# Optimization experiments

Hardware: AMD Instinct MI355X
Metric: run time of the kernel (lower is better)

## Reference

```python
import jax, jax.numpy as jnp
import numpy as np

TEMPERATURE = 1.0  # init kwarg
B, D = 8192, 128


def setup_inputs() -> dict:
    key = jax.random.key(0)
    k1, k2 = jax.random.split(key)
    sk = jax.random.normal(k1, (B, D), dtype=jnp.float32)
    im = jax.random.normal(k2, (B, D), dtype=jnp.float32)
    return {"sk": sk, "im": im}


def reference(sk, im):
    # The torch module builds a [2B,2B] Euclidean distance matrix over the
    # interleaved [sk_0, im_0, sk_1, im_1, ...] rows, then via the eye-mask /
    # repeat_interleave / [:,1::2] / good_indices / [::2] gather chain selects,
    # for each anchor i, logits row = [-d(sk_i, im_i)/T] ++ [-d(sk_i, im_j)/T, j != i]
    # with label 0, followed by mean cross-entropy.  Since cross-entropy only
    # depends on {row values} and which entry is positive, this is exactly:
    #   loss = mean_i( logsumexp_j(-d(sk_i, im_j)/T) - (-d(sk_i, im_i)/T) )
    # so we only need the [B,B] sk-vs-im distance block (dist_type == 0).
    sq = (
        jnp.sum(sk * sk, axis=1)[:, None]
        + jnp.sum(im * im, axis=1)[None, :]
        - 2.0 * (sk @ im.T)
    )  # [B, B] squared distances
    d = jnp.sqrt(jnp.maximum(sq, 0.0))
    logits = -d / TEMPERATURE  # [B, B]
    lse = jax.nn.logsumexp(logits, axis=1)  # [B]
    loss = jnp.mean(lse - jnp.diagonal(logits))
    return loss
```

## Files before the change

kernel.cpp:

```cpp
#include <hip/hip_runtime.h>
#include <math.h>

#define NB 8192
#define ND 128
#define GSTEP 64
#define NSTEP 8
#define NJB 16

#define C2F 2.0813689810056077f
#define NC2 (-4.1627379620112154f)

typedef float f32x4 __attribute__((ext_vector_type(4)));
typedef unsigned long long ull;

__global__ void __launch_bounds__(256) prep_kernel(
    const float* __restrict__ sk, const float* __restrict__ im,
    ull* __restrict__ skf, ull* __restrict__ imf,
    float* __restrict__ skn, float* __restrict__ imn,
    float* __restrict__ diag, float* __restrict__ gacc,
    unsigned* __restrict__ ticket) {
    if (blockIdx.x == 0 && threadIdx.x == 0) { *gacc = 0.f; *ticket = 0u; }
    const int gtid = blockIdx.x * 256 + threadIdx.x;
    const int row = gtid >> 4;
    const int j = gtid & 15;
    const size_t off = (size_t)row * ND + j * 8;
    const float4* a4 = reinterpret_cast<const float4*>(sk + off);
    const float4* b4 = reinterpret_cast<const float4*>(im + off);
    float4 a0 = a4[0], a1 = a4[1], b0 = b4[0], b1 = b4[1];

    unsigned al = 0, ah = 0, bl = 0, bh = 0;
    al = __builtin_amdgcn_cvt_pk_fp8_f32(a0.x, a0.y, al, false);
    al = __builtin_amdgcn_cvt_pk_fp8_f32(a0.z, a0.w, al, true);
    ah = __builtin_amdgcn_cvt_pk_fp8_f32(a1.x, a1.y, ah, false);
    ah = __builtin_amdgcn_cvt_pk_fp8_f32(a1.z, a1.w, ah, true);
    bl = __builtin_amdgcn_cvt_pk_fp8_f32(b0.x, b0.y, bl, false);
    bl = __builtin_amdgcn_cvt_pk_fp8_f32(b0.z, b0.w, bl, true);
    bh = __builtin_amdgcn_cvt_pk_fp8_f32(b1.x, b1.y, bh, false);
    bh = __builtin_amdgcn_cvt_pk_fp8_f32(b1.z, b1.w, bh, true);

    const size_t didx = (size_t)(row >> 4) * 256 + (j >> 2) * 64 + (j & 3) * 16 + (row & 15);
    skf[didx] = (ull)al | ((ull)ah << 32);
    imf[didx] = (ull)bl | ((ull)bh << 32);

    float sa = a0.x*a0.x + a0.y*a0.y + a0.z*a0.z + a0.w*a0.w
             + a1.x*a1.x + a1.y*a1.y + a1.z*a1.z + a1.w*a1.w;
    float sb = b0.x*b0.x + b0.y*b0.y + b0.z*b0.z + b0.w*b0.w
             + b1.x*b1.x + b1.y*b1.y + b1.z*b1.z + b1.w*b1.w;
    float d0 = a0.x-b0.x, d1 = a0.y-b0.y, d2 = a0.z-b0.z, d3 = a0.w-b0.w;
    float d4 = a1.x-b1.x, d5 = a1.y-b1.y, d6 = a1.z-b1.z, d7 = a1.w-b1.w;
    float sd = d0*d0 + d1*d1 + d2*d2 + d3*d3 + d4*d4 + d5*d5 + d6*d6 + d7*d7;
#pragma unroll
    for (int st = 1; st < 16; st <<= 1) {
        sa += __shfl_xor(sa, st);
        sb += __shfl_xor(sb, st);
        sd += __shfl_xor(sd, st);
    }
    if (j == 0) {
        skn[row] = sa * C2F;
        imn[row] = sb * C2F;
        diag[row] = sqrtf(sd);
    }
}

__global__ void __launch_bounds__(256, 4) tile_kernel(
    const ull* __restrict__ skf, const ull* __restrict__ imf,
    const float* __restrict__ skn, const float* __restrict__ imn,
    float* __restrict__ partial) {
    const int w = threadIdx.x >> 6, lane = threadIdx.x & 63;
    const int hi = lane >> 4, lo = lane & 15;
    const int gw = blockIdx.x * 4 + w;
    const int iw = (gw & 255) * 32;
    const int jgrp = gw >> 8;
    const int jg0 = jgrp * (GSTEP * NSTEP);

    long bfr[2][4];
    const int gi = iw >> 4;
#pragma unroll
    for (int n = 0; n < 2; ++n)
#pragma unroll
        for (int kk = 0; kk < 4; ++kk)
            bfr[n][kk] = (long)skf[(size_t)(gi + n) * 256 + kk * 64 + lane];
    float skv[2];
#pragma unroll
    for (int n = 0; n < 2; ++n) skv[n] = skn[iw + n * 16 + lo];

    float sacc[2] = {0.f, 0.f};

    for (int s = 0; s < NSTEP; ++s) {
        const int jb = jg0 + s * GSTEP;
        const size_t ga = (size_t)(jb >> 4) * 256;

        float imnv[4][4];
#pragma unroll
        for (int m = 0; m < 4; ++m) {
            float4 v = *reinterpret_cast<const float4*>(imn + jb + m * 16 + hi * 4);
            imnv[m][0] = v.x; imnv[m][1] = v.y; imnv[m][2] = v.z; imnv[m][3] = v.w;
        }

        f32x4 acc[4][2];
#pragma unroll
        for (int m = 0; m < 4; ++m)
#pragma unroll
            for (int n = 0; n < 2; ++n)
                acc[m][n] = (f32x4){0.f, 0.f, 0.f, 0.f};

#pragma unroll
        for (int kk = 0; kk < 4; ++kk) {
            long af[4];
#pragma unroll
            for (int m = 0; m < 4; ++m)
                af[m] = (long)imf[ga + (size_t)m * 256 + kk * 64 + lane];
#pragma unroll
            for (int m = 0; m < 4; ++m)
#pragma unroll
                for (int n = 0; n < 2; ++n)
                    acc[m][n] = __builtin_amdgcn_mfma_f32_16x16x32_fp8_fp8(
                        af[m], bfr[n][kk], acc[m][n], 0, 0, 0);
        }

#pragma unroll
        for (int n = 0; n < 2; ++n) {
            float ssum = 0.f;
#pragma unroll
            for (int m = 0; m < 4; ++m) {
#pragma unroll
                for (int r = 0; r < 4; ++r) {
                    float sq2 = fmaf(NC2, acc[m][n][r], skv[n]) + imnv[m][r];
                    float d2;
                    asm("v_sqrt_f32 %0, abs(%1)" : "=v"(d2) : "v"(sq2));
                    float e;
                    asm("v_exp_f32 %0, -%1" : "=v"(e) : "v"(d2));
                    ssum += e;
                }
            }
            sacc[n] += ssum;
        }
    }

#pragma unroll
    for (int n = 0; n < 2; ++n) {
        sacc[n] += __shfl_xor(sacc[n], 16);
        sacc[n] += __shfl_xor(sacc[n], 32);
    }
    if (lane < 16) {
        partial[(size_t)jgrp * NB + iw + lo] = sacc[0];
        partial[(size_t)jgrp * NB + iw + 16 + lo] = sacc[1];
    }
}

__global__ void finalize_kernel(const float* __restrict__ partial,
                                const float* __restrict__ diag,
                                float* __restrict__ gacc, unsigned* __restrict__ ticket,
                                float* __restrict__ out) {
    const int i = blockIdx.x * 256 + threadIdx.x;
    float rs = 0.f;
#pragma unroll
    for (int c = 0; c < NJB; ++c) rs += partial[(size_t)c * NB + i];
    float v = __logf(rs) + diag[i];
    __shared__ float red[256];
    red[threadIdx.x] = v;
    __syncthreads();
    for (int st = 128; st > 0; st >>= 1) {
        if (threadIdx.x < st) red[threadIdx.x] += red[threadIdx.x + st];
        __syncthreads();
    }
    if (threadIdx.x == 0) {
        atomicAdd(gacc, red[0]);
        __threadfence();
        unsigned old = atomicAdd(ticket, 1u);
        if (old == (NB / 256) - 1) {
            float tot = atomicAdd(gacc, 0.f);
            out[0] = tot / (float)NB;
        }
    }
}

extern "C" void kernel_launch(void* const* d_in, const int* in_sizes, int n_in,
                              void* d_out, int out_size, void* d_ws, size_t ws_size,
                              hipStream_t stream) {
    const float* sk = (const float*)d_in[0];
    const float* im = (const float*)d_in[1];
    float* out = (float*)d_out;
    float* ws = (float*)d_ws;

    ull* skf = (ull*)ws;
    ull* imf = skf + (size_t)NB * ND / 8;
    float* fbase   = ws + (size_t)NB * ND / 2;
    float* skn     = fbase;
    float* imn     = fbase + NB;
    float* diag    = fbase + 2 * NB;
    float* partial = fbase + 3 * NB;
    float* gacc    = partial + (size_t)NJB * NB;
    unsigned* ticket = (unsigned*)(gacc + 1);

    prep_kernel<<<NB * 16 / 256, 256, 0, stream>>>(
        sk, im, skf, imf, skn, imn, diag, gacc, ticket);
    tile_kernel<<<1024, 256, 0, stream>>>(skf, imf, skn, imn, partial);
    finalize_kernel<<<NB / 256, 256, 0, stream>>>(partial, diag, gacc, ticket, out);
}
```

Baseline: 87.51 us.

## Use bit-trick exp, prefetch fp8 tiles, and fuse finalize into tile kernel

The hardware v_exp_f32 in the inner epilogue is replaced by a Schraudolph-style approximation: an FMA followed by an int-to-float bit reinterpretation. This takes work off the transcendental unit, which also has to run a sqrt for every element, at the cost of a few percent error per exp term. The kernel now double-buffers the im fp8 fragment loads so the next k-slice or step is fetched during the MFMAs, and it staggers each wave's starting j-step. The separate finalize kernel is removed: row sums are accumulated with global atomics, and the last block, found by a ticket, computes the log-sum and the mean.

Result: slower. 109.1 us (+24.6%).

```diff
diff --git a/kernel.cpp b/kernel.cpp
--- a/kernel.cpp
+++ b/kernel.cpp
@@ -9,6 +9,8 @@
 
 #define C2F 2.0813689810056077f
 #define NC2 (-4.1627379620112154f)
+#define SCH_A (-8388608.0f)
+#define SCH_B 1064870050.0f
 
 typedef float f32x4 __attribute__((ext_vector_type(4)));
 typedef unsigned long long ull;
@@ -17,9 +19,9 @@
     const float* __restrict__ sk, const float* __restrict__ im,
     ull* __restrict__ skf, ull* __restrict__ imf,
     float* __restrict__ skn, float* __restrict__ imn,
-    float* __restrict__ diag, float* __restrict__ gacc,
+    float* __restrict__ diag, float* __restrict__ rowsum,
     unsigned* __restrict__ ticket) {
-    if (blockIdx.x == 0 && threadIdx.x == 0) { *gacc = 0.f; *ticket = 0u; }
+    if (blockIdx.x == 0 && threadIdx.x == 0) *ticket = 0u;
     const int gtid = blockIdx.x * 256 + threadIdx.x;
     const int row = gtid >> 4;
     const int j = gtid & 15;
@@ -59,19 +61,23 @@
         skn[row] = sa * C2F;
         imn[row] = sb * C2F;
         diag[row] = sqrtf(sd);
+    } else if (j == 1) {
+        rowsum[row] = 0.f;
     }
 }
 
 __global__ void __launch_bounds__(256, 4) tile_kernel(
     const ull* __restrict__ skf, const ull* __restrict__ imf,
     const float* __restrict__ skn, const float* __restrict__ imn,
-    float* __restrict__ partial) {
+    const float* __restrict__ diag, float* __restrict__ rowsum,
+    unsigned* __restrict__ ticket, float* __restrict__ out) {
     const int w = threadIdx.x >> 6, lane = threadIdx.x & 63;
     const int hi = lane >> 4, lo = lane & 15;
     const int gw = blockIdx.x * 4 + w;
     const int iw = (gw & 255) * 32;
     const int jgrp = gw >> 8;
-    const int jg0 = jgrp * (GSTEP * NSTEP);
+    const int phase = (w << 1) & (NSTEP - 1);
+    const size_t gbase = (size_t)jgrp * 8192;
 
     long bfr[2][4];
     const int gi = iw >> 4;
@@ -81,14 +87,22 @@
         for (int kk = 0; kk < 4; ++kk)
             bfr[n][kk] = (long)skf[(size_t)(gi + n) * 256 + kk * 64 + lane];
     float skv[2];
-#pragma unroll
-    for (int n = 0; n < 2; ++n) skv[n] = skn[iw + n * 16 + lo];
+    skv[0] = skn[iw + lo];
+    skv[1] = skn[iw + 16 + lo];
 
     float sacc[2] = {0.f, 0.f};
 
-    for (int s = 0; s < NSTEP; ++s) {
-        const int jb = jg0 + s * GSTEP;
-        const size_t ga = (size_t)(jb >> 4) * 256;
+    long af[2][4];
+#pragma unroll
+    for (int m = 0; m < 4; ++m)
+        af[0][m] = (long)imf[gbase + (size_t)phase * 1024 + (size_t)m * 256 + lane];
+
+    for (int s0 = 0; s0 < NSTEP; ++s0) {
+        const int s = (s0 + phase) & (NSTEP - 1);
+        const int sn = (s0 + 1 + phase) & (NSTEP - 1);
+        const int jb = jgrp * (GSTEP * NSTEP) + s * GSTEP;
+        const size_t ga = gbase + (size_t)s * 1024;
+        const size_t gan = gbase + (size_t)sn * 1024;
 
         float imnv[4][4];
 #pragma unroll
@@ -106,16 +120,17 @@
 
 #pragma unroll
         for (int kk = 0; kk < 4; ++kk) {
-            long af[4];
+            const int cur = kk & 1, nxt = cur ^ 1;
+            const size_t pga = (kk < 3) ? (ga + (size_t)(kk + 1) * 64) : gan;
 #pragma unroll
             for (int m = 0; m < 4; ++m)
-                af[m] = (long)imf[ga + (size_t)m * 256 + kk * 64 + lane];
+                af[nxt][m] = (long)imf[pga + (size_t)m * 256 + lane];
 #pragma unroll
             for (int m = 0; m < 4; ++m)
 #pragma unroll
                 for (int n = 0; n < 2; ++n)
                     acc[m][n] = __builtin_amdgcn_mfma_f32_16x16x32_fp8_fp8(
-                        af[m], bfr[n][kk], acc[m][n], 0, 0, 0);
+                        af[cur][m], bfr[n][kk], acc[m][n], 0, 0, 0);
         }
 
 #pragma unroll
@@ -128,8 +143,8 @@
                     float sq2 = fmaf(NC2, acc[m][n][r], skv[n]) + imnv[m][r];
                     float d2;
                     asm("v_sqrt_f32 %0, abs(%1)" : "=v"(d2) : "v"(sq2));
-                    float e;
-                    asm("v_exp_f32 %0, -%1" : "=v"(e) : "v"(d2));
+                    float tt = fmaf(d2, SCH_A, SCH_B);
+                    float e = __int_as_float((int)tt);
                     ssum += e;
                 }
             }
@@ -143,35 +158,32 @@
         sacc[n] += __shfl_xor(sacc[n], 32);
     }
     if (lane < 16) {
-        partial[(size_t)jgrp * NB + iw + lo] = sacc[0];
-        partial[(size_t)jgrp * NB + iw + 16 + lo] = sacc[1];
-    }
-}
-
-__global__ void finalize_kernel(const float* __restrict__ partial,
-                                const float* __restrict__ diag,
-                                float* __restrict__ gacc, unsigned* __restrict__ ticket,
-                                float* __restrict__ out) {
-    const int i = blockIdx.x * 256 + threadIdx.x;
-    float rs = 0.f;
-#pragma unroll
-    for (int c = 0; c < NJB; ++c) rs += partial[(size_t)c * NB + i];
-    float v = __logf(rs) + diag[i];
+        atomicAdd(&rowsum[iw + lo], sacc[0]);
+        atomicAdd(&rowsum[iw + 16 + lo], sacc[1]);
+    }
+
+    __shared__ unsigned lastFlag;
     __shared__ float red[256];
-    red[threadIdx.x] = v;
     __syncthreads();
-    for (int st = 128; st > 0; st >>= 1) {
-        if (threadIdx.x < st) red[threadIdx.x] += red[threadIdx.x + st];
+    if (threadIdx.x == 0) {
+        __threadfence();
+        lastFlag = (atomicAdd(ticket, 1u) == (unsigned)(gridDim.x - 1)) ? 1u : 0u;
+    }
+    __syncthreads();
+    if (lastFlag) {
+        __threadfence();
+        float s = 0.f;
+        for (int r = threadIdx.x; r < NB; r += 256) {
+            float rs = atomicAdd(&rowsum[r], 0.0f);
+            s += __logf(rs) + diag[r];
+        }
+        red[threadIdx.x] = s;
         __syncthreads();
-    }
-    if (threadIdx.x == 0) {
-        atomicAdd(gacc, red[0]);
-        __threadfence();
-        unsigned old = atomicAdd(ticket, 1u);
-        if (old == (NB / 256) - 1) {
-            float tot = atomicAdd(gacc, 0.f);
-            out[0] = tot / (float)NB;
-        }
+        for (int st = 128; st > 0; st >>= 1) {
+            if (threadIdx.x < st) red[threadIdx.x] += red[threadIdx.x + st];
+            __syncthreads();
+        }
+        if (threadIdx.x == 0) out[0] = red[0] / (float)NB;
     }
 }
 
@@ -185,16 +197,15 @@
 
     ull* skf = (ull*)ws;
     ull* imf = skf + (size_t)NB * ND / 8;
-    float* fbase   = ws + (size_t)NB * ND / 2;
-    float* skn     = fbase;
-    float* imn     = fbase + NB;
-    float* diag    = fbase + 2 * NB;
-    float* partial = fbase + 3 * NB;
-    float* gacc    = partial + (size_t)NJB * NB;
-    unsigned* ticket = (unsigned*)(gacc + 1);
+    float* fbase  = ws + (size_t)NB * ND / 2;
+    float* skn    = fbase;
+    float* imn    = fbase + NB;
+    float* diag   = fbase + 2 * NB;
+    float* rowsum = fbase + 3 * NB;
+    unsigned* ticket = (unsigned*)(fbase + 4 * NB);
 
     prep_kernel<<<NB * 16 / 256, 256, 0, stream>>>(
-        sk, im, skf, imf, skn, imn, diag, gacc, ticket);
-    tile_kernel<<<1024, 256, 0, stream>>>(skf, imf, skn, imn, partial);
-    finalize_kernel<<<NB / 256, 256, 0, stream>>>(partial, diag, gacc, ticket, out);
+        sk, im, skf, imf, skn, imn, diag, rowsum, ticket);
+    tile_kernel<<<1024, 256, 0, stream>>>(
+        skf, imf, skn, imn, diag, rowsum, ticket, out);
 }
```
